# Optimization experiments

Hardware: AMD Instinct MI355X
Metric: run time of the kernel (lower is better)

## Reference

```python
import jax, jax.numpy as jnp
import numpy as np

D = 1024      # model_dim
DK = 1024     # keys_dim
DV = 1024     # values_dim
H = 16        # heads
HDK = DK // H # per-head key dim (64)
HDV = DV // H
FF = 2048     # FFN default hidden_dim
EPS = 1e-5


def setup_inputs() -> dict:
    key = jax.random.key(0)
    ks = jax.random.split(key, 16)
    s = lambda k, sh, fan: jax.random.normal(k, sh, jnp.float32) * (1.0 / np.sqrt(fan))
    return {
        "x": jax.random.normal(ks[0], (8, 1024, D), jnp.float32),
        # per-head projections stored as [D, H, hd] (concat of the H small Linears)
        "Wq": s(ks[1], (D, H, HDK), D), "bq": jnp.zeros((H, HDK), jnp.float32),
        "Wk": s(ks[2], (D, H, HDK), D), "bk": jnp.zeros((H, HDK), jnp.float32),
        "Wv": s(ks[3], (D, H, HDV), D), "bv": jnp.zeros((H, HDV), jnp.float32),
        "Wo": s(ks[4], (DV, D), DV), "bo": jnp.zeros((D,), jnp.float32),
        "ln1_g": jnp.ones((D,), jnp.float32), "ln1_b": jnp.zeros((D,), jnp.float32),
        "W1": s(ks[5], (D, FF), D), "b1": jnp.zeros((FF,), jnp.float32),
        "W2": s(ks[6], (FF, D), FF), "b2": jnp.zeros((D,), jnp.float32),
        "ln2_g": jnp.ones((D,), jnp.float32), "ln2_b": jnp.zeros((D,), jnp.float32),
    }


def layer_norm(x, g, b):
    mu = jnp.mean(x, axis=-1, keepdims=True)
    var = jnp.mean(jnp.square(x - mu), axis=-1, keepdims=True)
    return (x - mu) * jax.lax.rsqrt(var + EPS) * g + b


def reference(x, Wq, bq, Wk, bk, Wv, bv, Wo, bo, ln1_g, ln1_b, W1, b1, W2, b2, ln2_g, ln2_b):
    # per-head projections (equivalent to H small Linears, batched)
    q = jnp.einsum("bsd,dhk->bhsk", x, Wq) + bq[:, None, :]
    k = jnp.einsum("bsd,dhk->bhsk", x, Wk) + bk[:, None, :]
    v = jnp.einsum("bsd,dhv->bhsv", x, Wv) + bv[:, None, :]
    # scaled dot-product attention per head (scale uses per-head dk)
    scores = jnp.einsum("bhsk,bhtk->bhst", q, k) / jnp.sqrt(jnp.float32(HDK))
    w = jax.nn.softmax(scores, axis=-1)
    ctx = jnp.einsum("bhst,bhtv->bhsv", w, v)           # [B,H,S,hdv]
    B, _, S, _ = ctx.shape
    ctx = ctx.transpose(0, 2, 1, 3).reshape(B, S, DV)   # concat heads
    c = ctx @ Wo + bo
    h = layer_norm(x + c, ln1_g, ln1_b)
    y = jax.nn.relu(h @ W1 + b1) @ W2 + b2
    return layer_norm(h + y, ln2_g, ln2_b)
```

## Files before the change

### kernel.cpp

```cpp
#include <hip/hip_runtime.h>
#include <hip/hip_bf16.h>
#include <cstdint>

typedef __bf16 bf16_t;
typedef __bf16 bf16x8 __attribute__((ext_vector_type(8)));
typedef __bf16 bf16x4 __attribute__((ext_vector_type(4)));
typedef float f32x4 __attribute__((ext_vector_type(4)));

#define SEQ    1024
#define BATCH  8
#define NTOK   8192
#define DMODEL 1024
#define NHEAD  16
#define HD     64
#define FFDIM  2048

__device__ __forceinline__ void async16(const void* g, void* l) {
  __builtin_amdgcn_global_load_lds(
      (const __attribute__((address_space(1))) void*)g,
      (__attribute__((address_space(3))) void*)l, 16, 0, 0);
}

__device__ __forceinline__ uint32_t pack2bf(float a, float b) {
  union { bf16_t h[2]; uint32_t u; } t;
  t.h[0] = (bf16_t)a; t.h[1] = (bf16_t)b;
  return t.u;
}

__global__ __launch_bounds__(256)
void cast_bf16_kernel(const float* __restrict__ in, bf16_t* __restrict__ out, int n4) {
  int i = blockIdx.x * 256 + threadIdx.x;
  if (i >= n4) return;
  float4 v = ((const float4*)in)[i];
  bf16x4 o = { (bf16_t)v.x, (bf16_t)v.y, (bf16_t)v.z, (bf16_t)v.w };
  *(bf16x4*)&out[(size_t)i * 4] = o;
}

__global__ __launch_bounds__(256)
void transpose_cast_kernel(const float* __restrict__ W, bf16_t* __restrict__ Wt,
                           int R, int C) {
  __shared__ float tile[32][33];
  const int bx = blockIdx.x * 32;
  const int by = blockIdx.y * 32;
  const int tx = threadIdx.x;
  const int ty = threadIdx.y;
#pragma unroll
  for (int i = 0; i < 4; ++i)
    tile[ty + 8 * i][tx] = W[(size_t)(by + ty + 8 * i) * C + bx + tx];
  __syncthreads();
#pragma unroll
  for (int i = 0; i < 4; ++i)
    Wt[(size_t)(bx + ty + 8 * i) * R + by + tx] = (bf16_t)tile[tx][ty + 8 * i];
}

template <int EPI>
__global__ __launch_bounds__(256, 4)
void gemm_bt(const bf16_t* __restrict__ A, const bf16_t* __restrict__ Bt,
             const float* __restrict__ bias0, const float* __restrict__ bias1,
             const float* __restrict__ bias2,
             const float* __restrict__ residF, const bf16_t* __restrict__ residB,
             void* __restrict__ o0, void* __restrict__ o1, void* __restrict__ o2,
             int K, int ldo, float qscale) {
  __shared__ bf16_t As[8192];
  __shared__ bf16_t Bs[8192];
  const int tid = threadIdx.x, w = tid >> 6, l = tid & 63;
  const int fr = l & 15, kg = (l >> 4) * 8;
  const int bm = blockIdx.x << 7, bn = blockIdx.y << 7;
  const int wr = (w >> 1) * 64, wc = (w & 1) * 64;

  const int srow = l >> 3;
  const int scol = ((l & 7) ^ srow) * 8;
  const int xork = (fr & 7) << 3;

  f32x4 acc[4][4];
#pragma unroll
  for (int i = 0; i < 4; ++i)
#pragma unroll
    for (int j = 0; j < 4; ++j) acc[i][j] = (f32x4){0.f, 0.f, 0.f, 0.f};

  const bf16_t* Ab = A + (size_t)bm * K;
  const bf16_t* Bb = Bt + (size_t)bn * K;

  const int nk = K >> 6;
  for (int kt = 0; kt < nk; ++kt) {
    const int k0 = kt << 6;
#pragma unroll
    for (int j = 0; j < 4; ++j) {
      const int ch = w * 4 + j;
      const int row = ch * 8 + srow;
      async16(Ab + (size_t)row * K + k0 + scol, &As[ch * 512]);
      async16(Bb + (size_t)row * K + k0 + scol, &Bs[ch * 512]);
    }
    asm volatile("s_waitcnt vmcnt(0)" ::: "memory");
    __syncthreads();

#pragma unroll
    for (int kk = 0; kk < 2; ++kk) {
      bf16x8 a[4], b[4];
      const int ko = (kk * 32 + kg) ^ xork;
#pragma unroll
      for (int i = 0; i < 4; ++i)
        a[i] = *(const bf16x8*)&As[(wr + i * 16 + fr) * 64 + ko];
#pragma unroll
      for (int j = 0; j < 4; ++j)
        b[j] = *(const bf16x8*)&Bs[(wc + j * 16 + fr) * 64 + ko];
#pragma unroll
      for (int i = 0; i < 4; ++i)
#pragma unroll
        for (int j = 0; j < 4; ++j)
          acc[i][j] = __builtin_amdgcn_mfma_f32_16x16x32_bf16(a[i], b[j], acc[i][j], 0, 0, 0);
    }
    __syncthreads();
  }

  const int lr = (l >> 4) * 4, lc = fr;
#pragma unroll
  for (int j = 0; j < 4; ++j) {
    const int col = bn + wc + j * 16 + lc;
#pragma unroll
    for (int i = 0; i < 4; ++i) {
      if (EPI == 2 && (col >> 10) == 2) {
        const int cl = col & 1023, h_ = cl >> 6, e_ = cl & 63;
        const int row0 = bm + wr + i * 16 + lr;
        const int b_ = row0 >> 10, s_ = row0 & 1023;
        const float bv = bias2[cl];
        bf16x4 o = { (bf16_t)(acc[i][j][0] + bv), (bf16_t)(acc[i][j][1] + bv),
                     (bf16_t)(acc[i][j][2] + bv), (bf16_t)(acc[i][j][3] + bv) };
        *(bf16x4*)&((bf16_t*)o2)[((size_t)((b_ * NHEAD + h_) * HD + e_)) * SEQ + s_] = o;
        continue;
      }
#pragma unroll
      for (int r = 0; r < 4; ++r) {
        const int row = bm + wr + i * 16 + lr + r;
        const float v = acc[i][j][r];
        if (EPI == 0) {
          float o = v + bias0[col];
          if (residF) o += residF[(size_t)row * ldo + col];
          ((float*)o0)[(size_t)row * ldo + col] = o;
        } else if (EPI == 3) {
          const size_t idx = (size_t)row * ldo + col;
          ((float*)o0)[idx] = v + bias0[col] + (float)residB[idx];
        } else if (EPI == 1) {
          ((bf16_t*)o0)[(size_t)row * ldo + col] = (bf16_t)fmaxf(v + bias0[col], 0.f);
        } else {
          const int mode = col >> 10, cl = col & 1023;
          const int b_ = row >> 10, s_ = row & 1023, h_ = cl >> 6, e_ = cl & 63;
          if (mode == 0) {
            ((bf16_t*)o0)[((size_t)((b_ * NHEAD + h_) * SEQ + s_)) * HD + e_] =
                (bf16_t)((v + bias0[cl]) * qscale);
          } else {
            ((bf16_t*)o1)[((size_t)((b_ * NHEAD + h_) * SEQ + s_)) * HD + e_] =
                (bf16_t)(v + bias1[cl]);
          }
        }
      }
    }
  }
}

__global__ __launch_bounds__(256, 4)
void attn_kernel(const bf16_t* __restrict__ Q, const bf16_t* __restrict__ K,
                 const bf16_t* __restrict__ VT, bf16_t* __restrict__ CTX) {
  const int bh = blockIdx.x;
  const int qt = blockIdx.y * 128;
  const int b_ = bh >> 4, h_ = bh & 15;
  const bf16_t* qh = Q + (size_t)bh * SEQ * HD;
  const bf16_t* kh = K + (size_t)bh * SEQ * HD;
  const bf16_t* vh = VT + (size_t)bh * HD * SEQ;
  const int tid = threadIdx.x, wave = tid >> 6, lane = tid & 63;
  const int fr = lane & 15, g = lane >> 4, kg = g * 8;

  __shared__ bf16_t Ks[2][64 * 64];
  __shared__ bf16_t Vs[2][64 * 64];

  const int srow = lane >> 3;
  const int scol = ((lane & 7) ^ srow) * 8;

  bf16x8 qf[2][2];
#pragma unroll
  for (int i = 0; i < 2; ++i)
#pragma unroll
    for (int kk = 0; kk < 2; ++kk)
      qf[i][kk] = *(const bf16x8*)&qh[(size_t)(qt + wave * 32 + i * 16 + fr) * HD + kk * 32 + kg];

  f32x4 octx[2][4];
  float mrun[2], lrun[2];
#pragma unroll
  for (int i = 0; i < 2; ++i) {
#pragma unroll
    for (int j = 0; j < 4; ++j) octx[i][j] = (f32x4){0.f, 0.f, 0.f, 0.f};
    mrun[i] = -1e30f; lrun[i] = 0.f;
  }

  auto stage = [&](int buf, int t) {
#pragma unroll
    for (int i = 0; i < 2; ++i) {
      const int ch = i * 4 + wave;
      const int row = ch * 8 + srow;
      async16(&kh[(size_t)(t * 64 + row) * HD + scol], &Ks[buf][ch * 512]);
      async16(&vh[(size_t)row * SEQ + t * 64 + scol], &Vs[buf][ch * 512]);
    }
  };

  stage(0, 0);
  asm volatile("s_waitcnt vmcnt(0)" ::: "memory");
  __syncthreads();

  const int srcA = fr + ((g & 1) << 5);
  const int srcB = srcA + 16;
  const bool ghi = (g >= 2);

  for (int t = 0; t < SEQ / 64; ++t) {
    const int cur = t & 1;
    if (t + 1 < SEQ / 64) stage(cur ^ 1, t + 1);

    f32x4 sc[2][4];
#pragma unroll
    for (int i = 0; i < 2; ++i)
#pragma unroll
      for (int j = 0; j < 4; ++j) sc[i][j] = (f32x4){0.f, 0.f, 0.f, 0.f};
#pragma unroll
    for (int kk = 0; kk < 2; ++kk) {
      bf16x8 kf[4];
#pragma unroll
      for (int j = 0; j < 4; ++j) {
        const int row = j * 16 + fr;
        kf[j] = *(const bf16x8*)&Ks[cur][row * 64 + ((kk * 32 + kg) ^ ((row & 7) << 3))];
      }
#pragma unroll
      for (int i = 0; i < 2; ++i)
#pragma unroll
        for (int j = 0; j < 4; ++j)
          sc[i][j] = __builtin_amdgcn_mfma_f32_16x16x32_bf16(kf[j], qf[i][kk], sc[i][j], 0, 0, 0);
    }

    float pmx[2];
    int ok = 1;
#pragma unroll
    for (int i = 0; i < 2; ++i) {
      float m0 = fmaxf(fmaxf(sc[i][0][0], sc[i][0][1]), fmaxf(sc[i][0][2], sc[i][0][3]));
      float m1 = fmaxf(fmaxf(sc[i][1][0], sc[i][1][1]), fmaxf(sc[i][1][2], sc[i][1][3]));
      float m2 = fmaxf(fmaxf(sc[i][2][0], sc[i][2][1]), fmaxf(sc[i][2][2], sc[i][2][3]));
      float m3 = fmaxf(fmaxf(sc[i][3][0], sc[i][3][1]), fmaxf(sc[i][3][2], sc[i][3][3]));
      pmx[i] = fmaxf(fmaxf(m0, m1), fmaxf(m2, m3));
      ok &= (pmx[i] <= mrun[i] + 8.f) ? 1 : 0;
    }
    if (!__all(ok)) {
#pragma unroll
      for (int i = 0; i < 2; ++i) {
        float mx = pmx[i];
        mx = fmaxf(mx, __shfl_xor(mx, 16));
        mx = fmaxf(mx, __shfl_xor(mx, 32));
        const float mnew = fmaxf(mrun[i], mx);
        const float alpha = exp2f(mrun[i] - mnew);
        mrun[i] = mnew;
        lrun[i] *= alpha;
#pragma unroll
        for (int j = 0; j < 4; ++j)
#pragma unroll
          for (int r = 0; r < 4; ++r) octx[i][j][r] *= alpha;
      }
    }
    uint32_t pk[2][4][2];
#pragma unroll
    for (int i = 0; i < 2; ++i) {
      const float m = mrun[i];
      float s = 0.f;
#pragma unroll
      for (int j = 0; j < 4; ++j) {
#pragma unroll
        for (int r = 0; r < 4; ++r) {
          const float p = exp2f(sc[i][j][r] - m);
          sc[i][j][r] = p;
          s += p;
        }
        pk[i][j][0] = pack2bf(sc[i][j][0], sc[i][j][1]);
        pk[i][j][1] = pack2bf(sc[i][j][2], sc[i][j][3]);
      }
      lrun[i] += s;
    }

#pragma unroll
    for (int kk2 = 0; kk2 < 2; ++kk2) {
      bf16x8 vf[4];
#pragma unroll
      for (int j2 = 0; j2 < 4; ++j2) {
        const int row = j2 * 16 + fr;
        vf[j2] = *(const bf16x8*)&Vs[cur][row * 64 + ((kk2 * 32 + kg) ^ ((row & 7) << 3))];
      }
      const int jlo = 2 * kk2, jhi = jlo + 1;
#pragma unroll
      for (int i = 0; i < 2; ++i) {
        const uint32_t aL0 = __shfl(pk[i][jlo][0], srcA), aL1 = __shfl(pk[i][jlo][1], srcA);
        const uint32_t bL0 = __shfl(pk[i][jlo][0], srcB), bL1 = __shfl(pk[i][jlo][1], srcB);
        const uint32_t aH0 = __shfl(pk[i][jhi][0], srcA), aH1 = __shfl(pk[i][jhi][1], srcA);
        const uint32_t bH0 = __shfl(pk[i][jhi][0], srcB), bH1 = __shfl(pk[i][jhi][1], srcB);
        union { bf16x8 v; uint32_t u[4]; } pf;
        pf.u[0] = ghi ? aH0 : aL0;
        pf.u[1] = ghi ? aH1 : aL1;
        pf.u[2] = ghi ? bH0 : bL0;
        pf.u[3] = ghi ? bH1 : bL1;
#pragma unroll
        for (int j2 = 0; j2 < 4; ++j2)
          octx[i][j2] = __builtin_amdgcn_mfma_f32_16x16x32_bf16(vf[j2], pf.v, octx[i][j2], 0, 0, 0);
      }
    }

    asm volatile("s_waitcnt vmcnt(0)" ::: "memory");
    __syncthreads();
  }

#pragma unroll
  for (int i = 0; i < 2; ++i) {
    float lsum = lrun[i];
    lsum += __shfl_xor(lsum, 16);
    lsum += __shfl_xor(lsum, 32);
    const float inv = 1.f / lsum;
    const int row = qt + wave * 32 + i * 16 + fr;
    const size_t base = ((size_t)(b_ * SEQ + row)) * DMODEL + h_ * HD;
#pragma unroll
    for (int j2 = 0; j2 < 4; ++j2) {
      bf16x4 o = { (bf16_t)(octx[i][j2][0] * inv), (bf16_t)(octx[i][j2][1] * inv),
                   (bf16_t)(octx[i][j2][2] * inv), (bf16_t)(octx[i][j2][3] * inv) };
      *(bf16x4*)&CTX[base + j2 * 16 + g * 4] = o;
    }
  }
}

template <int OUTB>
__global__ __launch_bounds__(256)
void ln_kernel(const float* __restrict__ Y, const float* __restrict__ g,
               const float* __restrict__ b, void* __restrict__ outp) {
  const int row = blockIdx.x, tid = threadIdx.x;
  const int wave = tid >> 6, lane = tid & 63;
  const float4 yv = ((const float4*)Y)[(size_t)row * 256 + tid];
  const float s0 = yv.x, s1 = yv.y, s2 = yv.z, s3 = yv.w;
  float sum = s0 + s1 + s2 + s3;
  float sq = s0 * s0 + s1 * s1 + s2 * s2 + s3 * s3;
#pragma unroll
  for (int off = 1; off < 64; off <<= 1) {
    sum += __shfl_xor(sum, off);
    sq += __shfl_xor(sq, off);
  }
  __shared__ float red[8];
  if (lane == 0) { red[wave] = sum; red[4 + wave] = sq; }
  __syncthreads();
  sum = red[0] + red[1] + red[2] + red[3];
  sq = red[4] + red[5] + red[6] + red[7];
  const float mu = sum * (1.f / 1024.f);
  const float var = sq * (1.f / 1024.f) - mu * mu;
  const float rstd = rsqrtf(var + 1e-5f);
  const float4 gv = ((const float4*)g)[tid];
  const float4 bv = ((const float4*)b)[tid];
  const float o0 = (s0 - mu) * rstd * gv.x + bv.x;
  const float o1 = (s1 - mu) * rstd * gv.y + bv.y;
  const float o2 = (s2 - mu) * rstd * gv.z + bv.z;
  const float o3 = (s3 - mu) * rstd * gv.w + bv.w;
  if (OUTB) {
    bf16x4 ob = { (bf16_t)o0, (bf16_t)o1, (bf16_t)o2, (bf16_t)o3 };
    *(bf16x4*)&((bf16_t*)outp)[(size_t)row * 1024 + tid * 4] = ob;
  } else {
    ((float4*)outp)[(size_t)row * 256 + tid] = make_float4(o0, o1, o2, o3);
  }
}

extern "C" void kernel_launch(void* const* d_in, const int* in_sizes, int n_in,
                              void* d_out, int out_size, void* d_ws, size_t ws_size,
                              hipStream_t stream) {
  const float* x   = (const float*)d_in[0];
  const float* Wq  = (const float*)d_in[1];
  const float* bq  = (const float*)d_in[2];
  const float* Wk  = (const float*)d_in[3];
  const float* bk  = (const float*)d_in[4];
  const float* Wv  = (const float*)d_in[5];
  const float* bv  = (const float*)d_in[6];
  const float* Wo  = (const float*)d_in[7];
  const float* bo  = (const float*)d_in[8];
  const float* g1  = (const float*)d_in[9];
  const float* be1 = (const float*)d_in[10];
  const float* W1  = (const float*)d_in[11];
  const float* b1  = (const float*)d_in[12];
  const float* W2  = (const float*)d_in[13];
  const float* b2  = (const float*)d_in[14];
  const float* g2  = (const float*)d_in[15];
  const float* be2 = (const float*)d_in[16];

  char* ws = (char*)d_ws;
  const size_t MB = 1u << 20;
  bf16_t* xb    = (bf16_t*)(ws + 0 * MB);
  bf16_t* WqkvT = (bf16_t*)(ws + 16 * MB);
  bf16_t* WoT   = (bf16_t*)(ws + 22 * MB);
  bf16_t* W1T   = (bf16_t*)(ws + 24 * MB);
  bf16_t* W2T   = (bf16_t*)(ws + 28 * MB);
  bf16_t* qb    = (bf16_t*)(ws + 32 * MB);
  bf16_t* kb    = (bf16_t*)(ws + 48 * MB);
  bf16_t* vT    = (bf16_t*)(ws + 64 * MB);
  float*  y0    = (float*)(ws + 80 * MB);
  bf16_t* ctx = xb;
  bf16_t* hb  = qb;
  bf16_t* u   = kb;

  cast_bf16_kernel<<<dim3(NTOK * DMODEL / 4 / 256), dim3(256), 0, stream>>>(x, xb, NTOK * DMODEL / 4);
  transpose_cast_kernel<<<dim3(32, 32), dim3(32, 8), 0, stream>>>(Wq, WqkvT, 1024, 1024);
  transpose_cast_kernel<<<dim3(32, 32), dim3(32, 8), 0, stream>>>(Wk, WqkvT + 1024 * 1024, 1024, 1024);
  transpose_cast_kernel<<<dim3(32, 32), dim3(32, 8), 0, stream>>>(Wv, WqkvT + 2 * 1024 * 1024, 1024, 1024);
  transpose_cast_kernel<<<dim3(32, 32), dim3(32, 8), 0, stream>>>(Wo, WoT, 1024, 1024);
  transpose_cast_kernel<<<dim3(64, 32), dim3(32, 8), 0, stream>>>(W1, W1T, 1024, 2048);
  transpose_cast_kernel<<<dim3(32, 64), dim3(32, 8), 0, stream>>>(W2, W2T, 2048, 1024);

  const float qscale = 0.125f * 1.44269504088896f;

  gemm_bt<2><<<dim3(64, 24), dim3(256), 0, stream>>>(
      xb, WqkvT, bq, bk, bv, nullptr, nullptr, qb, kb, vT, 1024, 0, qscale);

  attn_kernel<<<dim3(128, 8), dim3(256), 0, stream>>>(qb, kb, vT, ctx);

  gemm_bt<0><<<dim3(64, 8), dim3(256), 0, stream>>>(
      ctx, WoT, bo, nullptr, nullptr, x, nullptr, y0, nullptr, nullptr, 1024, 1024, 1.f);

  ln_kernel<1><<<dim3(NTOK), dim3(256), 0, stream>>>(y0, g1, be1, hb);

  gemm_bt<1><<<dim3(64, 16), dim3(256), 0, stream>>>(
      hb, W1T, b1, nullptr, nullptr, nullptr, nullptr, u, nullptr, nullptr, 1024, 2048, 1.f);

  gemm_bt<3><<<dim3(64, 8), dim3(256), 0, stream>>>(
      u, W2T, b2, nullptr, nullptr, nullptr, hb, y0, nullptr, nullptr, 2048, 1024, 1.f);

  ln_kernel<0><<<dim3(NTOK), dim3(256), 0, stream>>>(y0, g2, be2, (float*)d_out);
}
```

Measured before the change: 322.8 us.

## Merge weight transposes into one launch, remap attention blocks per XCD, load V directly

The six weight transpose-cast launches become one kernel that reads a per-matrix table to find its tile. The attention grid is flattened and remapped so all query tiles of a (batch, head) pair land on the same XCD, which should improve L2 reuse of K and V. V fragments are now read straight from global memory into registers at the top of each iteration instead of being staged through LDS, which halves LDS use but puts global-load latency on the PV path.

```diff
diff --git a/kernel.cpp b/kernel.cpp
--- a/kernel.cpp
+++ b/kernel.cpp
@@ -36,21 +36,35 @@
   *(bf16x4*)&out[(size_t)i * 4] = o;
 }
 
+struct TransTab {
+  const float* src[6];
+  bf16_t* dst[6];
+  int R[6], C[6];
+  int tile0[7];
+};
+
 __global__ __launch_bounds__(256)
-void transpose_cast_kernel(const float* __restrict__ W, bf16_t* __restrict__ Wt,
-                           int R, int C) {
+void transpose_cast_all(TransTab tab) {
   __shared__ float tile[32][33];
-  const int bx = blockIdx.x * 32;
-  const int by = blockIdx.y * 32;
-  const int tx = threadIdx.x;
-  const int ty = threadIdx.y;
+  const int b = blockIdx.x;
+  int m = 0;
+#pragma unroll
+  for (int k = 0; k < 5; ++k) m += (b >= tab.tile0[k + 1]) ? 1 : 0;
+  const int t = b - tab.tile0[m];
+  const int C = tab.C[m], R = tab.R[m];
+  const int ntx = C >> 5;
+  const int ty = t / ntx, tx = t - ty * ntx;
+  const float* W = tab.src[m];
+  bf16_t* Wt = tab.dst[m];
+  const int bx = tx * 32, by = ty * 32;
+  const int lx = threadIdx.x & 31, ly = threadIdx.x >> 5;
 #pragma unroll
   for (int i = 0; i < 4; ++i)
-    tile[ty + 8 * i][tx] = W[(size_t)(by + ty + 8 * i) * C + bx + tx];
+    tile[ly + 8 * i][lx] = W[(size_t)(by + ly + 8 * i) * C + bx + lx];
   __syncthreads();
 #pragma unroll
   for (int i = 0; i < 4; ++i)
-    Wt[(size_t)(bx + ty + 8 * i) * R + by + tx] = (bf16_t)tile[tx][ty + 8 * i];
+    Wt[(size_t)(bx + ly + 8 * i) * R + by + lx] = (bf16_t)tile[lx][ly + 8 * i];
 }
 
 template <int EPI>
@@ -161,8 +175,10 @@
 __global__ __launch_bounds__(256, 4)
 void attn_kernel(const bf16_t* __restrict__ Q, const bf16_t* __restrict__ K,
                  const bf16_t* __restrict__ VT, bf16_t* __restrict__ CTX) {
-  const int bh = blockIdx.x;
-  const int qt = blockIdx.y * 128;
+  const int bid = blockIdx.x;
+  const int xcd = bid & 7, slot = bid >> 3;
+  const int bh = xcd * 16 + (slot & 15);
+  const int qt = (slot >> 4) * 128;
   const int b_ = bh >> 4, h_ = bh & 15;
   const bf16_t* qh = Q + (size_t)bh * SEQ * HD;
   const bf16_t* kh = K + (size_t)bh * SEQ * HD;
@@ -171,7 +187,6 @@
   const int fr = lane & 15, g = lane >> 4, kg = g * 8;
 
   __shared__ bf16_t Ks[2][64 * 64];
-  __shared__ bf16_t Vs[2][64 * 64];
 
   const int srow = lane >> 3;
   const int scol = ((lane & 7) ^ srow) * 8;
@@ -192,17 +207,16 @@
     mrun[i] = -1e30f; lrun[i] = 0.f;
   }
 
-  auto stage = [&](int buf, int t) {
+  auto stageK = [&](int buf, int t) {
 #pragma unroll
     for (int i = 0; i < 2; ++i) {
       const int ch = i * 4 + wave;
       const int row = ch * 8 + srow;
       async16(&kh[(size_t)(t * 64 + row) * HD + scol], &Ks[buf][ch * 512]);
-      async16(&vh[(size_t)row * SEQ + t * 64 + scol], &Vs[buf][ch * 512]);
     }
   };
 
-  stage(0, 0);
+  stageK(0, 0);
   asm volatile("s_waitcnt vmcnt(0)" ::: "memory");
   __syncthreads();
 
@@ -212,7 +226,15 @@
 
   for (int t = 0; t < SEQ / 64; ++t) {
     const int cur = t & 1;
-    if (t + 1 < SEQ / 64) stage(cur ^ 1, t + 1);
+
+    bf16x8 vf[2][4];
+#pragma unroll
+    for (int kk2 = 0; kk2 < 2; ++kk2)
+#pragma unroll
+      for (int j2 = 0; j2 < 4; ++j2)
+        vf[kk2][j2] = *(const bf16x8*)&vh[(size_t)(j2 * 16 + fr) * SEQ + t * 64 + kk2 * 32 + kg];
+
+    if (t + 1 < SEQ / 64) stageK(cur ^ 1, t + 1);
 
     f32x4 sc[2][4];
 #pragma unroll
@@ -282,12 +304,6 @@
 
 #pragma unroll
     for (int kk2 = 0; kk2 < 2; ++kk2) {
-      bf16x8 vf[4];
-#pragma unroll
-      for (int j2 = 0; j2 < 4; ++j2) {
-        const int row = j2 * 16 + fr;
-        vf[j2] = *(const bf16x8*)&Vs[cur][row * 64 + ((kk2 * 32 + kg) ^ ((row & 7) << 3))];
-      }
       const int jlo = 2 * kk2, jhi = jlo + 1;
 #pragma unroll
       for (int i = 0; i < 2; ++i) {
@@ -302,7 +318,7 @@
         pf.u[3] = ghi ? bH1 : bL1;
 #pragma unroll
         for (int j2 = 0; j2 < 4; ++j2)
-          octx[i][j2] = __builtin_amdgcn_mfma_f32_16x16x32_bf16(vf[j2], pf.v, octx[i][j2], 0, 0, 0);
+          octx[i][j2] = __builtin_amdgcn_mfma_f32_16x16x32_bf16(vf[kk2][j2], pf.v, octx[i][j2], 0, 0, 0);
       }
     }
 
@@ -401,19 +417,24 @@
   bf16_t* u   = kb;
 
   cast_bf16_kernel<<<dim3(NTOK * DMODEL / 4 / 256), dim3(256), 0, stream>>>(x, xb, NTOK * DMODEL / 4);
-  transpose_cast_kernel<<<dim3(32, 32), dim3(32, 8), 0, stream>>>(Wq, WqkvT, 1024, 1024);
-  transpose_cast_kernel<<<dim3(32, 32), dim3(32, 8), 0, stream>>>(Wk, WqkvT + 1024 * 1024, 1024, 1024);
-  transpose_cast_kernel<<<dim3(32, 32), dim3(32, 8), 0, stream>>>(Wv, WqkvT + 2 * 1024 * 1024, 1024, 1024);
-  transpose_cast_kernel<<<dim3(32, 32), dim3(32, 8), 0, stream>>>(Wo, WoT, 1024, 1024);
-  transpose_cast_kernel<<<dim3(64, 32), dim3(32, 8), 0, stream>>>(W1, W1T, 1024, 2048);
-  transpose_cast_kernel<<<dim3(32, 64), dim3(32, 8), 0, stream>>>(W2, W2T, 2048, 1024);
+  TransTab tab;
+  tab.src[0] = Wq;  tab.dst[0] = WqkvT;                 tab.R[0] = 1024; tab.C[0] = 1024;
+  tab.src[1] = Wk;  tab.dst[1] = WqkvT + 1024 * 1024;   tab.R[1] = 1024; tab.C[1] = 1024;
+  tab.src[2] = Wv;  tab.dst[2] = WqkvT + 2 * 1024 * 1024; tab.R[2] = 1024; tab.C[2] = 1024;
+  tab.src[3] = Wo;  tab.dst[3] = WoT;                   tab.R[3] = 1024; tab.C[3] = 1024;
+  tab.src[4] = W1;  tab.dst[4] = W1T;                   tab.R[4] = 1024; tab.C[4] = 2048;
+  tab.src[5] = W2;  tab.dst[5] = W2T;                   tab.R[5] = 2048; tab.C[5] = 1024;
+  tab.tile0[0] = 0;    tab.tile0[1] = 1024; tab.tile0[2] = 2048;
+  tab.tile0[3] = 3072; tab.tile0[4] = 4096; tab.tile0[5] = 6144;
+  tab.tile0[6] = 8192;
+  transpose_cast_all<<<dim3(8192), dim3(256), 0, stream>>>(tab);
 
   const float qscale = 0.125f * 1.44269504088896f;
 
   gemm_bt<2><<<dim3(64, 24), dim3(256), 0, stream>>>(
       xb, WqkvT, bq, bk, bv, nullptr, nullptr, qb, kb, vT, 1024, 0, qscale);
 
-  attn_kernel<<<dim3(128, 8), dim3(256), 0, stream>>>(qb, kb, vT, ctx);
+  attn_kernel<<<dim3(1024), dim3(256), 0, stream>>>(qb, kb, vT, ctx);
 
   gemm_bt<0><<<dim3(64, 8), dim3(256), 0, stream>>>(
       ctx, WoT, bo, nullptr, nullptr, x, nullptr, y0, nullptr, nullptr, 1024, 1024, 1.f);
```

New measurement: 369.2 us. +14.4%, slower.
